# Optimization experiments

Hardware: AMD Instinct MI355X
Metric: run time of the kernel (lower is better)

## Reference

```python
import jax, jax.numpy as jnp
import numpy as np

EPS = 1e-6


def setup_inputs() -> dict:
    key = jax.random.key(0)
    k1, k2, k3, k4 = jax.random.split(key, 4)
    B, N, D = 8, 4096, 512
    x = jax.random.normal(k1, (B, N, D), dtype=jnp.float32)
    # torch nn.Linear(dim, 3*dim, bias=False): weight shape [3D, D], y = x @ W.T
    w_qkv = jax.random.normal(k2, (3 * D, D), dtype=jnp.float32) * (1.0 / np.sqrt(D))
    w_proj = jax.random.normal(k3, (D, D), dtype=jnp.float32) * (1.0 / np.sqrt(D))
    b_proj = jax.random.normal(k4, (D,), dtype=jnp.float32) * 0.01
    return {"x": x, "w_qkv": w_qkv, "w_proj": w_proj, "b_proj": b_proj, "heads": 8}


def reference(x, w_qkv, w_proj, b_proj, heads):
    B, N, D = x.shape
    H = heads
    d = D // H
    # qkv projection -> (3, B, H, N, d)
    qkv = (x @ w_qkv.T).reshape(B, N, 3, H, d).transpose(2, 0, 3, 1, 4)
    q, k, v = qkv[0], qkv[1], qkv[2]
    # elu+1 feature map (positive features)
    q = jax.nn.elu(q) + 1.0 + EPS
    k = jax.nn.elu(k) + 1.0 + EPS
    # kv summary: [B,H,d,d]
    kv = jnp.einsum('bhnd,bhne->bhde', k, v)
    # denominator: q . sum_n(k) -> [B,H,N]
    denom = jnp.einsum('bhnd,bhd->bhn', q, k.sum(axis=2))
    out = jnp.einsum('bhnd,bhde->bhne', q, kv) / (denom[..., None] + EPS)
    out = out.transpose(0, 2, 1, 3).reshape(B, N, D)
    return out @ w_proj.T + b_proj
```

## Files before the change

### kernel.cpp

```cpp
#include <hip/hip_runtime.h>
#include <hip/hip_bf16.h>
#include <math.h>

#define EPSF 1e-6f

constexpr int Bc = 8;
constexpr int Nc = 4096;
constexpr int Dc = 512;
constexpr int QKVC = 3 * Dc;

typedef __attribute__((ext_vector_type(8))) short short8v;
typedef __attribute__((ext_vector_type(8))) unsigned short ushort8v;
typedef __attribute__((ext_vector_type(4))) float float4v;

__device__ __forceinline__ unsigned short f2bf(float f) {
    union { float f; unsigned int u; } v; v.f = f;
    unsigned int u = v.u;
    return (unsigned short)((u + 0x7fffu + ((u >> 16) & 1u)) >> 16);
}
__device__ __forceinline__ float bf2f(unsigned short h) {
    union { unsigned int u; float f; } v; v.u = ((unsigned int)h) << 16;
    return v.f;
}

typedef __attribute__((address_space(1))) const void gvoid_t;
typedef __attribute__((address_space(3))) void lvoid_t;
__device__ __forceinline__ void llds16(const void* g, void* l) {
    __builtin_amdgcn_global_load_lds((gvoid_t*)g, (lvoid_t*)l, 16, 0, 0);
}

__global__ __launch_bounds__(256) void cvt_f32_bf16(
    const float* __restrict__ in, unsigned short* __restrict__ out, int n8)
{
    int i = blockIdx.x * 256 + threadIdx.x;
    if (i >= n8) return;
    float4 a = reinterpret_cast<const float4*>(in)[2 * i];
    float4 b = reinterpret_cast<const float4*>(in)[2 * i + 1];
    ushort8v o;
    o[0] = f2bf(a.x); o[1] = f2bf(a.y); o[2] = f2bf(a.z); o[3] = f2bf(a.w);
    o[4] = f2bf(b.x); o[5] = f2bf(b.y); o[6] = f2bf(b.z); o[7] = f2bf(b.w);
    reinterpret_cast<ushort8v*>(out)[i] = o;
}

template <int ELU_COLS, bool BIAS, bool OUT_BF16>
__global__ __launch_bounds__(256) void gemm_bf16(
    const unsigned short* __restrict__ A, int lda,
    const unsigned short* __restrict__ Bm, int ldb,
    void* __restrict__ Cout, int ldc, int K,
    const float* __restrict__ bias)
{
    __shared__ unsigned short lA[2][128 * 32];
    __shared__ unsigned short lB[2][128 * 32];

    const int t    = threadIdx.x;
    const int bm   = blockIdx.x * 128;
    const int bn   = blockIdx.y * 128;
    const int w    = t >> 6, lane = t & 63;
    const int ln   = lane & 15, g = lane >> 4;
    const int wr   = (w >> 1) * 64, wc = (w & 1) * 64;

    const int r0  = t >> 2;
    const int ks0 = (t & 3) * 8;
    const unsigned short* Ap0 = A + (size_t)(bm + r0) * lda + ks0;
    const unsigned short* Ap1 = A + (size_t)(bm + r0 + 64) * lda + ks0;
    const unsigned short* Bp0 = Bm + (size_t)(bn + r0) * ldb + ks0;
    const unsigned short* Bp1 = Bm + (size_t)(bn + r0 + 64) * ldb + ks0;

    float4v acc[4][4];
#pragma unroll
    for (int i = 0; i < 4; ++i)
#pragma unroll
        for (int j = 0; j < 4; ++j) acc[i][j] = {0.f, 0.f, 0.f, 0.f};

    const int nt = K >> 5;

#define STAGE_T(buf, k0) do { \
        llds16(Ap0 + (k0), lA[buf] + (size_t)t * 8); \
        llds16(Ap1 + (k0), lA[buf] + (size_t)(t + 256) * 8); \
        llds16(Bp0 + (k0), lB[buf] + (size_t)t * 8); \
        llds16(Bp1 + (k0), lB[buf] + (size_t)(t + 256) * 8); \
    } while (0)

    STAGE_T(0, 0);
    __syncthreads();

    int cur = 0;
    for (int tt = 0; tt < nt; ++tt) {
        if (tt + 1 < nt) STAGE_T(cur ^ 1, (tt + 1) << 5);

        const unsigned short* pa = lA[cur];
        const unsigned short* pb = lB[cur];
        short8v a[4], b[4];
#pragma unroll
        for (int i = 0; i < 4; ++i)
            a[i] = *reinterpret_cast<const short8v*>(pa + (wr + i * 16 + ln) * 32 + g * 8);
#pragma unroll
        for (int j = 0; j < 4; ++j)
            b[j] = *reinterpret_cast<const short8v*>(pb + (wc + j * 16 + ln) * 32 + g * 8);

        __builtin_amdgcn_s_setprio(1);
#pragma unroll
        for (int i = 0; i < 4; ++i)
#pragma unroll
            for (int j = 0; j < 4; ++j)
                acc[i][j] = __builtin_amdgcn_mfma_f32_16x16x32_bf16(a[i], b[j], acc[i][j], 0, 0, 0);
        __builtin_amdgcn_s_setprio(0);

        __syncthreads();
        cur ^= 1;
    }
#undef STAGE_T

#pragma unroll
    for (int i = 0; i < 4; ++i) {
        const int Rb = bm + wr + i * 16 + g * 4;
#pragma unroll
        for (int j = 0; j < 4; ++j) {
            const int Cc = bn + wc + j * 16 + ln;
            const bool do_elu = (ELU_COLS > 0) && (Cc < ELU_COLS);
            float bv = BIAS ? bias[Cc] : 0.f;
#pragma unroll
            for (int r = 0; r < 4; ++r) {
                float v = acc[i][j][r];
                if (do_elu) v = (v > 0.f) ? (v + 1.0f + EPSF) : (expf(v) + EPSF);
                if (BIAS) v += bv;
                if (OUT_BF16)
                    ((unsigned short*)Cout)[(size_t)(Rb + r) * ldc + Cc] = f2bf(v);
                else
                    ((float*)Cout)[(size_t)(Rb + r) * ldc + Cc] = v;
            }
        }
    }
}

__global__ __launch_bounds__(256) void kv_part(
    const unsigned short* __restrict__ qkv,
    float* __restrict__ kvp, float* __restrict__ ksp)
{
    const int bh = blockIdx.x, chunk = blockIdx.y;
    const int b = bh >> 3, h = bh & 7;

    __shared__ float kt[64][68];
    __shared__ float vt[64][68];
    __shared__ float ksl[4][64];

    const int t  = threadIdx.x;
    const int e  = t & 63, dg = t >> 6;
    const int rr = t >> 3, slot = t & 7;

    float acc[16] = {};
    float ks = 0.f;

    const size_t base = ((size_t)b * Nc + (size_t)chunk * 512) * QKVC + h * 64;

    for (int n0 = 0; n0 < 512; n0 += 64) {
#pragma unroll
        for (int half = 0; half < 2; ++half) {
            const int row = rr + half * 32;
            const unsigned short* kr = qkv + base + (size_t)(n0 + row) * QKVC + Dc + slot * 8;
            const unsigned short* vr = kr + Dc;
            ushort8v kq = *reinterpret_cast<const ushort8v*>(kr);
            ushort8v vq = *reinterpret_cast<const ushort8v*>(vr);
            float4 k0 = make_float4(bf2f(kq[0]), bf2f(kq[1]), bf2f(kq[2]), bf2f(kq[3]));
            float4 k1 = make_float4(bf2f(kq[4]), bf2f(kq[5]), bf2f(kq[6]), bf2f(kq[7]));
            float4 v0 = make_float4(bf2f(vq[0]), bf2f(vq[1]), bf2f(vq[2]), bf2f(vq[3]));
            float4 v1 = make_float4(bf2f(vq[4]), bf2f(vq[5]), bf2f(vq[6]), bf2f(vq[7]));
            *reinterpret_cast<float4*>(&kt[row][slot * 8])     = k0;
            *reinterpret_cast<float4*>(&kt[row][slot * 8 + 4]) = k1;
            *reinterpret_cast<float4*>(&vt[row][slot * 8])     = v0;
            *reinterpret_cast<float4*>(&vt[row][slot * 8 + 4]) = v1;
        }
        __syncthreads();
#pragma unroll 2
        for (int nn = 0; nn < 64; ++nn) {
            const float vv = vt[nn][e];
            const float4 q0 = *reinterpret_cast<const float4*>(&kt[nn][dg * 16]);
            const float4 q1 = *reinterpret_cast<const float4*>(&kt[nn][dg * 16 + 4]);
            const float4 q2 = *reinterpret_cast<const float4*>(&kt[nn][dg * 16 + 8]);
            const float4 q3 = *reinterpret_cast<const float4*>(&kt[nn][dg * 16 + 12]);
            acc[0]  += q0.x * vv; acc[1]  += q0.y * vv; acc[2]  += q0.z * vv; acc[3]  += q0.w * vv;
            acc[4]  += q1.x * vv; acc[5]  += q1.y * vv; acc[6]  += q1.z * vv; acc[7]  += q1.w * vv;
            acc[8]  += q2.x * vv; acc[9]  += q2.y * vv; acc[10] += q2.z * vv; acc[11] += q2.w * vv;
            acc[12] += q3.x * vv; acc[13] += q3.y * vv; acc[14] += q3.z * vv; acc[15] += q3.w * vv;
        }
#pragma unroll
        for (int nn = 0; nn < 16; ++nn) ks += kt[dg * 16 + nn][e];
        __syncthreads();
    }

    float* kvpp = kvp + ((size_t)bh * 8 + chunk) * 4096;
#pragma unroll
    for (int i = 0; i < 16; ++i) kvpp[(dg * 16 + i) * 64 + e] = acc[i];

    ksl[dg][e] = ks;
    __syncthreads();
    if (t < 64) ksp[((size_t)bh * 8 + chunk) * 64 + t] =
        ksl[0][t] + ksl[1][t] + ksl[2][t] + ksl[3][t];
}

__global__ __launch_bounds__(256) void kv_reduce(
    const float* __restrict__ kvp, const float* __restrict__ ksp,
    unsigned short* __restrict__ kvT, float* __restrict__ ksum)
{
    const int bh = blockIdx.x, t = threadIdx.x;
    const float* src = kvp + (size_t)bh * 8 * 4096;
#pragma unroll
    for (int i = 0; i < 16; ++i) {
        const int idx = i * 256 + t;
        float s = 0.f;
#pragma unroll
        for (int c = 0; c < 8; ++c) s += src[c * 4096 + idx];
        const int d = idx >> 6, e = idx & 63;
        kvT[(size_t)bh * 4096 + e * 64 + d] = f2bf(s);
    }
    if (t < 64) {
        float s = 0.f;
#pragma unroll
        for (int c = 0; c < 8; ++c) s += ksp[((size_t)bh * 8 + c) * 64 + t];
        ksum[bh * 64 + t] = s;
    }
}

__global__ __launch_bounds__(256) void attn_mfma(
    unsigned short* __restrict__ qkv, const unsigned short* __restrict__ kvT,
    const float* __restrict__ ksum)
{
    const int bh = blockIdx.x;
    const int mt = blockIdx.y;
    const int b = bh >> 3, h = bh & 7;

    __shared__ unsigned short qs[128][72];
    __shared__ unsigned short kvs[64][72];
    __shared__ float dn[128];
    __shared__ float kss[64];

    const int t = threadIdx.x;
    unsigned short* qbase = qkv + ((size_t)b * Nc + (size_t)mt * 128) * QKVC + h * 64;

#pragma unroll
    for (int s = 0; s < 4; ++s) {
        const int c = t + 256 * s;
        const int row = c >> 3, sl = c & 7;
        ushort8v qv = *reinterpret_cast<const ushort8v*>(qbase + (size_t)row * QKVC + sl * 8);
        *reinterpret_cast<ushort8v*>(&qs[row][sl * 8]) = qv;
    }
    const unsigned short* kvbase = kvT + (size_t)bh * 4096;
#pragma unroll
    for (int s = 0; s < 2; ++s) {
        const int c = t + 256 * s;
        const int e = c >> 3, sl = c & 7;
        ushort8v v = *reinterpret_cast<const ushort8v*>(kvbase + e * 64 + sl * 8);
        *reinterpret_cast<ushort8v*>(&kvs[e][sl * 8]) = v;
    }
    if (t < 64) kss[t] = ksum[bh * 64 + t];
    __syncthreads();

    if (t < 128) {
        float s = EPSF;
#pragma unroll
        for (int d = 0; d < 64; ++d) s += bf2f(qs[t][d]) * kss[d];
        dn[t] = 1.0f / s;
    }
    __syncthreads();

    const int w = t >> 6, lane = t & 63;
    const int ln = lane & 15, g = lane >> 4;

    float4v acc[2][4];
#pragma unroll
    for (int i = 0; i < 2; ++i)
#pragma unroll
        for (int j = 0; j < 4; ++j) acc[i][j] = {0.f, 0.f, 0.f, 0.f};

    short8v a[2][2], bf[4][2];
#pragma unroll
    for (int i = 0; i < 2; ++i)
#pragma unroll
        for (int kk = 0; kk < 2; ++kk)
            a[i][kk] = *reinterpret_cast<const short8v*>(&qs[w * 32 + i * 16 + ln][kk * 32 + g * 8]);
#pragma unroll
    for (int j = 0; j < 4; ++j)
#pragma unroll
        for (int kk = 0; kk < 2; ++kk)
            bf[j][kk] = *reinterpret_cast<const short8v*>(&kvs[j * 16 + ln][kk * 32 + g * 8]);

#pragma unroll
    for (int kk = 0; kk < 2; ++kk)
#pragma unroll
        for (int i = 0; i < 2; ++i)
#pragma unroll
            for (int j = 0; j < 4; ++j)
                acc[i][j] = __builtin_amdgcn_mfma_f32_16x16x32_bf16(a[i][kk], bf[j][kk], acc[i][j], 0, 0, 0);

#pragma unroll
    for (int i = 0; i < 2; ++i) {
        const int lrow = w * 32 + i * 16 + g * 4;
#pragma unroll
        for (int j = 0; j < 4; ++j) {
            const int e = j * 16 + ln;
#pragma unroll
            for (int r = 0; r < 4; ++r) {
                float v = acc[i][j][r] * dn[lrow + r];
                qbase[(size_t)(lrow + r) * QKVC + e] = f2bf(v);
            }
        }
    }
}

extern "C" void kernel_launch(void* const* d_in, const int* in_sizes, int n_in,
                              void* d_out, int out_size, void* d_ws, size_t ws_size,
                              hipStream_t stream)
{
    const float* x      = (const float*)d_in[0];
    const float* w_qkv  = (const float*)d_in[1];
    const float* w_proj = (const float*)d_in[2];
    const float* b_proj = (const float*)d_in[3];
    float* out = (float*)d_out;

    char* ws = (char*)d_ws;
    unsigned short* qkvb = (unsigned short*)ws;
    size_t off = (size_t)32768 * 1536 * 2;
    unsigned short* xb   = (unsigned short*)(ws + off); off += (size_t)32768 * 512 * 2;
    unsigned short* wqb  = (unsigned short*)(ws + off); off += (size_t)1536 * 512 * 2;
    unsigned short* wpb  = (unsigned short*)(ws + off); off += (size_t)512 * 512 * 2;
    float* kvp           = (float*)(ws + off);          off += (size_t)64 * 8 * 4096 * 4;
    float* ksp           = (float*)(ws + off);          off += (size_t)64 * 8 * 64 * 4;
    unsigned short* kvT  = (unsigned short*)(ws + off); off += (size_t)64 * 4096 * 2;
    float* ksumb         = (float*)(ws + off);

    cvt_f32_bf16<<<dim3((32768 * 512 / 8 + 255) / 256), dim3(256), 0, stream>>>(x, xb, 32768 * 512 / 8);
    cvt_f32_bf16<<<dim3((1536 * 512 / 8 + 255) / 256), dim3(256), 0, stream>>>(w_qkv, wqb, 1536 * 512 / 8);
    cvt_f32_bf16<<<dim3((512 * 512 / 8 + 255) / 256), dim3(256), 0, stream>>>(w_proj, wpb, 512 * 512 / 8);

    gemm_bf16<1024, false, true><<<dim3(256, 12), dim3(256), 0, stream>>>(
        xb, Dc, wqb, Dc, qkvb, QKVC, Dc, nullptr);

    kv_part<<<dim3(64, 8), dim3(256), 0, stream>>>(qkvb, kvp, ksp);
    kv_reduce<<<dim3(64), dim3(256), 0, stream>>>(kvp, ksp, kvT, ksumb);

    attn_mfma<<<dim3(64, 32), dim3(256), 0, stream>>>(qkvb, kvT, ksumb);

    gemm_bf16<0, true, false><<<dim3(256, 4), dim3(256), 0, stream>>>(
        qkvb, QKVC, wpb, Dc, out, Dc, Dc, b_proj);
}
```

Measured before the change: 203.0 us.

## Fuse attention output computation with output projection GEMM

Replaces the separate attention-apply kernel and the output-projection GEMM with one kernel. For each 128-row by 128-column output tile it loops over the heads, computes q·kv and the normalizer in registers, stages the normalized bf16 result in swizzled LDS, and accumulates the projection with MFMA. This removes the write-back of the attention output into the qkv buffer and its re-read by the projection GEMM. The cost is that each of the 4 column blocks recomputes the per-head attention product, and every head iteration adds extra syncthreads.

```diff
diff --git a/kernel.cpp b/kernel.cpp
--- a/kernel.cpp
+++ b/kernel.cpp
@@ -221,88 +221,170 @@
     }
 }
 
-__global__ __launch_bounds__(256) void attn_mfma(
-    unsigned short* __restrict__ qkv, const unsigned short* __restrict__ kvT,
-    const float* __restrict__ ksum)
-{
-    const int bh = blockIdx.x;
-    const int mt = blockIdx.y;
-    const int b = bh >> 3, h = bh & 7;
-
-    __shared__ unsigned short qs[128][72];
-    __shared__ unsigned short kvs[64][72];
-    __shared__ float dn[128];
-    __shared__ float kss[64];
+__global__ __launch_bounds__(256) void attn_proj(
+    const unsigned short* __restrict__ qkv,
+    const unsigned short* __restrict__ kvT,
+    const float* __restrict__ ksum,
+    const unsigned short* __restrict__ wp,
+    const float* __restrict__ bias,
+    float* __restrict__ out)
+{
+    __shared__ unsigned short lq[128 * 64];
+    __shared__ unsigned short lkv[64 * 64];
+    __shared__ unsigned short lwp[128 * 64];
+    __shared__ unsigned short loL[128 * 64];
 
     const int t = threadIdx.x;
-    unsigned short* qbase = qkv + ((size_t)b * Nc + (size_t)mt * 128) * QKVC + h * 64;
-
-#pragma unroll
-    for (int s = 0; s < 4; ++s) {
-        const int c = t + 256 * s;
-        const int row = c >> 3, sl = c & 7;
-        ushort8v qv = *reinterpret_cast<const ushort8v*>(qbase + (size_t)row * QKVC + sl * 8);
-        *reinterpret_cast<ushort8v*>(&qs[row][sl * 8]) = qv;
-    }
-    const unsigned short* kvbase = kvT + (size_t)bh * 4096;
-#pragma unroll
-    for (int s = 0; s < 2; ++s) {
-        const int c = t + 256 * s;
-        const int e = c >> 3, sl = c & 7;
-        ushort8v v = *reinterpret_cast<const ushort8v*>(kvbase + e * 64 + sl * 8);
-        *reinterpret_cast<ushort8v*>(&kvs[e][sl * 8]) = v;
-    }
-    if (t < 64) kss[t] = ksum[bh * 64 + t];
-    __syncthreads();
-
-    if (t < 128) {
-        float s = EPSF;
-#pragma unroll
-        for (int d = 0; d < 64; ++d) s += bf2f(qs[t][d]) * kss[d];
-        dn[t] = 1.0f / s;
-    }
-    __syncthreads();
+    const int rowBlk = blockIdx.x;
+    const int bn = blockIdx.y;
+    const int b = rowBlk >> 5;
+    const size_t rowBase = (size_t)rowBlk * 128;
 
     const int w = t >> 6, lane = t & 63;
     const int ln = lane & 15, g = lane >> 4;
-
-    float4v acc[2][4];
-#pragma unroll
-    for (int i = 0; i < 2; ++i)
-#pragma unroll
-        for (int j = 0; j < 4; ++j) acc[i][j] = {0.f, 0.f, 0.f, 0.f};
-
-    short8v a[2][2], bf[4][2];
-#pragma unroll
-    for (int i = 0; i < 2; ++i)
+    const int wr = (w >> 1) * 64, wc = (w & 1) * 64;
+    const int l7 = ln & 7;
+
+    char* lqc  = (char*)lq;
+    char* lkvc = (char*)lkv;
+    char* lwpc = (char*)lwp;
+    char* loLc = (char*)loL;
+
+    float4v accP[4][4];
+#pragma unroll
+    for (int i = 0; i < 4; ++i)
+#pragma unroll
+        for (int j = 0; j < 4; ++j) accP[i][j] = {0.f, 0.f, 0.f, 0.f};
+
+    for (int h = 0; h < 8; ++h) {
+        const int bh = b * 8 + h;
+        const unsigned short* qsrc = qkv + rowBase * QKVC + h * 64;
+        const unsigned short* wsrc = wp + (size_t)(bn * 128) * 512 + h * 64;
+        const unsigned short* ksrc = kvT + (size_t)bh * 4096;
+
+#pragma unroll
+        for (int s = 0; s < 4; ++s) {
+            const int c = s * 256 + t, r = c >> 3, ci = c & 7;
+            ushort8v qv = *reinterpret_cast<const ushort8v*>(qsrc + (size_t)r * QKVC + ci * 8);
+            *reinterpret_cast<ushort8v*>(lqc + r * 128 + ((ci ^ (r & 7)) << 4)) = qv;
+            ushort8v wv = *reinterpret_cast<const ushort8v*>(wsrc + (size_t)r * 512 + ci * 8);
+            *reinterpret_cast<ushort8v*>(lwpc + r * 128 + ((ci ^ (r & 7)) << 4)) = wv;
+        }
+#pragma unroll
+        for (int s = 0; s < 2; ++s) {
+            const int c = s * 256 + t, r = c >> 3, ci = c & 7;
+            ushort8v kvv = *reinterpret_cast<const ushort8v*>(ksrc + r * 64 + ci * 8);
+            *reinterpret_cast<ushort8v*>(lkvc + r * 128 + ((ci ^ (r & 7)) << 4)) = kvv;
+        }
+        __syncthreads();
+
+        float ksv[2][8];
+        {
+            const float* ksb = ksum + bh * 64 + g * 8;
+            float4 a0 = *reinterpret_cast<const float4*>(ksb);
+            float4 a1 = *reinterpret_cast<const float4*>(ksb + 4);
+            float4 b0 = *reinterpret_cast<const float4*>(ksb + 32);
+            float4 b1 = *reinterpret_cast<const float4*>(ksb + 36);
+            ksv[0][0] = a0.x; ksv[0][1] = a0.y; ksv[0][2] = a0.z; ksv[0][3] = a0.w;
+            ksv[0][4] = a1.x; ksv[0][5] = a1.y; ksv[0][6] = a1.z; ksv[0][7] = a1.w;
+            ksv[1][0] = b0.x; ksv[1][1] = b0.y; ksv[1][2] = b0.z; ksv[1][3] = b0.w;
+            ksv[1][4] = b1.x; ksv[1][5] = b1.y; ksv[1][6] = b1.z; ksv[1][7] = b1.w;
+        }
+
+        short8v akv[4][2], bq[2][2];
+#pragma unroll
+        for (int i = 0; i < 4; ++i)
+#pragma unroll
+            for (int kk = 0; kk < 2; ++kk)
+                akv[i][kk] = *reinterpret_cast<const short8v*>(
+                    lkvc + (i * 16 + ln) * 128 + (((kk * 4 + g) ^ l7) << 4));
+#pragma unroll
+        for (int j = 0; j < 2; ++j)
+#pragma unroll
+            for (int kk = 0; kk < 2; ++kk)
+                bq[j][kk] = *reinterpret_cast<const short8v*>(
+                    lqc + (w * 32 + j * 16 + ln) * 128 + (((kk * 4 + g) ^ l7) << 4));
+
+        float4v acco[4][2];
+#pragma unroll
+        for (int i = 0; i < 4; ++i)
+#pragma unroll
+            for (int j = 0; j < 2; ++j) acco[i][j] = {0.f, 0.f, 0.f, 0.f};
 #pragma unroll
         for (int kk = 0; kk < 2; ++kk)
-            a[i][kk] = *reinterpret_cast<const short8v*>(&qs[w * 32 + i * 16 + ln][kk * 32 + g * 8]);
-#pragma unroll
-    for (int j = 0; j < 4; ++j)
+#pragma unroll
+            for (int i = 0; i < 4; ++i)
+#pragma unroll
+                for (int j = 0; j < 2; ++j)
+                    acco[i][j] = __builtin_amdgcn_mfma_f32_16x16x32_bf16(
+                        akv[i][kk], bq[j][kk], acco[i][j], 0, 0, 0);
+
+        float inv[2];
+#pragma unroll
+        for (int j = 0; j < 2; ++j) {
+            float p = 0.f;
+#pragma unroll
+            for (int kk = 0; kk < 2; ++kk)
+#pragma unroll
+                for (int m = 0; m < 8; ++m)
+                    p += bf2f((unsigned short)bq[j][kk][m]) * ksv[kk][m];
+            p += __shfl_xor(p, 16);
+            p += __shfl_xor(p, 32);
+            inv[j] = 1.0f / (p + EPSF);
+        }
+
+#pragma unroll
+        for (int i = 0; i < 4; ++i)
+#pragma unroll
+            for (int j = 0; j < 2; ++j) {
+                unsigned int p0 = (unsigned int)f2bf(acco[i][j][0] * inv[j]) |
+                                  ((unsigned int)f2bf(acco[i][j][1] * inv[j]) << 16);
+                unsigned int p1 = (unsigned int)f2bf(acco[i][j][2] * inv[j]) |
+                                  ((unsigned int)f2bf(acco[i][j][3] * inv[j]) << 16);
+                const int row = w * 32 + j * 16 + ln;
+                const int chunk = i * 2 + (g >> 1);
+                char* dst = loLc + row * 128 + (((chunk ^ l7) << 4) | ((g & 1) << 3));
+                *reinterpret_cast<uint2*>(dst) = make_uint2(p0, p1);
+            }
+        __syncthreads();
+
+        short8v ao[4][2], bw[4][2];
+#pragma unroll
+        for (int i = 0; i < 4; ++i)
+#pragma unroll
+            for (int kk = 0; kk < 2; ++kk)
+                ao[i][kk] = *reinterpret_cast<const short8v*>(
+                    loLc + (wr + i * 16 + ln) * 128 + (((kk * 4 + g) ^ l7) << 4));
+#pragma unroll
+        for (int j = 0; j < 4; ++j)
+#pragma unroll
+            for (int kk = 0; kk < 2; ++kk)
+                bw[j][kk] = *reinterpret_cast<const short8v*>(
+                    lwpc + (wc + j * 16 + ln) * 128 + (((kk * 4 + g) ^ l7) << 4));
+
+        __builtin_amdgcn_s_setprio(1);
 #pragma unroll
         for (int kk = 0; kk < 2; ++kk)
-            bf[j][kk] = *reinterpret_cast<const short8v*>(&kvs[j * 16 + ln][kk * 32 + g * 8]);
-
-#pragma unroll
-    for (int kk = 0; kk < 2; ++kk)
-#pragma unroll
-        for (int i = 0; i < 2; ++i)
-#pragma unroll
-            for (int j = 0; j < 4; ++j)
-                acc[i][j] = __builtin_amdgcn_mfma_f32_16x16x32_bf16(a[i][kk], bf[j][kk], acc[i][j], 0, 0, 0);
-
-#pragma unroll
-    for (int i = 0; i < 2; ++i) {
-        const int lrow = w * 32 + i * 16 + g * 4;
-#pragma unroll
-        for (int j = 0; j < 4; ++j) {
-            const int e = j * 16 + ln;
-#pragma unroll
-            for (int r = 0; r < 4; ++r) {
-                float v = acc[i][j][r] * dn[lrow + r];
-                qbase[(size_t)(lrow + r) * QKVC + e] = f2bf(v);
-            }
+#pragma unroll
+            for (int i = 0; i < 4; ++i)
+#pragma unroll
+                for (int j = 0; j < 4; ++j)
+                    accP[i][j] = __builtin_amdgcn_mfma_f32_16x16x32_bf16(
+                        ao[i][kk], bw[j][kk], accP[i][j], 0, 0, 0);
+        __builtin_amdgcn_s_setprio(0);
+        __syncthreads();
+    }
+
+#pragma unroll
+    for (int j = 0; j < 4; ++j) {
+        const int col = bn * 128 + wc + j * 16 + ln;
+        const float bv = bias[col];
+#pragma unroll
+        for (int i = 0; i < 4; ++i) {
+            const size_t rg = rowBase + wr + i * 16 + g * 4;
+#pragma unroll
+            for (int rr = 0; rr < 4; ++rr)
+                out[(rg + rr) * 512 + col] = accP[i][j][rr] + bv;
         }
     }
 }
@@ -338,8 +420,6 @@
     kv_part<<<dim3(64, 8), dim3(256), 0, stream>>>(qkvb, kvp, ksp);
     kv_reduce<<<dim3(64), dim3(256), 0, stream>>>(kvp, ksp, kvT, ksumb);
 
-    attn_mfma<<<dim3(64, 32), dim3(256), 0, stream>>>(qkvb, kvT, ksumb);
-
-    gemm_bf16<0, true, false><<<dim3(256, 4), dim3(256), 0, stream>>>(
-        qkvb, QKVC, wpb, Dc, out, Dc, Dc, b_proj);
-}
+    attn_proj<<<dim3(256, 4), dim3(256), 0, stream>>>(
+        qkvb, kvT, ksumb, wpb, b_proj, out);
+}
```

Result: no change. 203.8 us (+0.4%).
